# Performance work log

Measured on AMD Instinct MI355X. Metric: run time of the kernel, lower is better.

Reference implementation:

```python
import jax, jax.numpy as jnp
import numpy as np
import math

B, T, C = 2, 4096, 768
NH = 12
HS = C // NH

def setup_inputs() -> dict:
    key = jax.random.key(0)
    k1, k2, k3 = jax.random.split(key, 3)
    x = jax.random.normal(k1, (B, T, C), dtype=jnp.float32)
    w_attn = jax.random.normal(k2, (C, 3 * C), dtype=jnp.float32) * (1.0 / math.sqrt(C))
    w_proj = jax.random.normal(k3, (C, C), dtype=jnp.float32) * (1.0 / math.sqrt(C))
    return {"x": x, "w_attn": w_attn, "w_proj": w_proj}

def reference(x, w_attn, w_proj):
    b, t, c = x.shape
    qkv = x @ w_attn                      # [b, t, 3c]
    q, k, v = jnp.split(qkv, 3, axis=-1)
    # [b, nh, t, hs]
    q = q.reshape(b, t, NH, HS).transpose(0, 2, 1, 3)
    k = k.reshape(b, t, NH, HS).transpose(0, 2, 1, 3)
    v = v.reshape(b, t, NH, HS).transpose(0, 2, 1, 3)
    scores = jnp.einsum('bhqd,bhkd->bhqk', q, k) / math.sqrt(HS)
    causal = jnp.tril(jnp.ones((t, t), dtype=bool))
    scores = jnp.where(causal[None, None], scores, -jnp.inf)
    att = jax.nn.softmax(scores, axis=-1)  # dropout p=0 -> identity
    out = jnp.einsum('bhqk,bhkd->bhqd', att, v)
    out = out.transpose(0, 2, 1, 3).reshape(b, t, c)
    return out @ w_proj
```

## Files before the change

### kernel.cpp

```cpp
#include <hip/hip_runtime.h>
#include <hip/hip_bf16.h>
#include <stdint.h>

#define NB 2
#define NT 4096
#define NC 768
#define NHEAD 12
#define HS 64
#define MTOK (NB * NT)
#define C3 (3 * NC)

typedef __bf16 bf16x8 __attribute__((ext_vector_type(8)));
typedef float f32x4 __attribute__((ext_vector_type(4)));
typedef float f32x16 __attribute__((ext_vector_type(16)));

#define KSCALE_LOG2E 0.18033688011f

__device__ __forceinline__ unsigned short f2bf(float f) {
  union { float f; uint32_t u; } v; v.f = f;
  uint32_t r = v.u + 0x7fffu + ((v.u >> 16) & 1u);
  return (unsigned short)(r >> 16);
}
__device__ __forceinline__ unsigned short bft(float f) {
  return (unsigned short)(__builtin_bit_cast(unsigned int, f) >> 16);
}
__device__ __forceinline__ uint32_t pack_bf2(float a, float b) {
  return (__builtin_bit_cast(uint32_t, b) & 0xffff0000u) |
         (__builtin_bit_cast(uint32_t, a) >> 16);
}

__device__ __forceinline__ void gload_lds16(const unsigned short* g, unsigned short* ldsbase) {
  __builtin_amdgcn_global_load_lds(
      (const __attribute__((address_space(1))) unsigned int*)g,
      (__attribute__((address_space(3))) unsigned int*)ldsbase, 16, 0, 0);
}

__device__ __forceinline__ f32x4 mfma16(bf16x8 a, bf16x8 b, f32x4 c) {
  return __builtin_amdgcn_mfma_f32_16x16x32_bf16(a, b, c, 0, 0, 0);
}
__device__ __forceinline__ f32x16 mfma32(bf16x8 a, bf16x8 b, f32x16 c) {
  return __builtin_amdgcn_mfma_f32_32x32x16_bf16(a, b, c, 0, 0, 0);
}

__global__ __launch_bounds__(256) void prep(
    const float* __restrict__ x, const float* __restrict__ wa, const float* __restrict__ wp,
    unsigned short* __restrict__ xb, unsigned short* __restrict__ waT,
    unsigned short* __restrict__ wpT) {
  const int bx = blockIdx.x;
  if (bx < 576) {
    __shared__ float tile[64][65];
    const float* src; unsigned short* dst;
    int srcN, dstN, k0, n0, qscale;
    if (bx < 432) {
      src = wa; dst = waT; srcN = C3; dstN = NC; qscale = 1;
      k0 = (bx / 36) * 64; n0 = (bx % 36) * 64;
    } else {
      const int t = bx - 432;
      src = wp; dst = wpT; srcN = NC; dstN = NC; qscale = 0;
      k0 = (t / 12) * 64; n0 = (t % 12) * 64;
    }
    const int tr = threadIdx.x >> 4;
    const int tc = (threadIdx.x & 15) * 4;
#pragma unroll
    for (int p = 0; p < 4; ++p) {
      const int r = p * 16 + tr;
      const float4 v = *reinterpret_cast<const float4*>(src + (size_t)(k0 + r) * srcN + n0 + tc);
      tile[r][tc + 0] = v.x; tile[r][tc + 1] = v.y;
      tile[r][tc + 2] = v.z; tile[r][tc + 3] = v.w;
    }
    __syncthreads();
#pragma unroll
    for (int p = 0; p < 4; ++p) {
      const int n = p * 16 + tr;
      const float sc = (qscale && (n0 + n) < NC) ? KSCALE_LOG2E : 1.0f;
      ushort4 o;
      o.x = f2bf(tile[tc + 0][n] * sc); o.y = f2bf(tile[tc + 1][n] * sc);
      o.z = f2bf(tile[tc + 2][n] * sc); o.w = f2bf(tile[tc + 3][n] * sc);
      *reinterpret_cast<ushort4*>(dst + (size_t)(n0 + n) * dstN + k0 + tc) = o;
    }
  } else {
    const int gid = (bx - 576) * 256 + threadIdx.x;
    const float4 v = reinterpret_cast<const float4*>(x)[gid];
    ushort4 o;
    o.x = f2bf(v.x); o.y = f2bf(v.y); o.z = f2bf(v.z); o.w = f2bf(v.w);
    reinterpret_cast<ushort4*>(xb)[gid] = o;
  }
}

template <int OUT_BF16>
__global__ __launch_bounds__(256) void gemm128(
    const unsigned short* __restrict__ A,
    const unsigned short* __restrict__ Bt,
    void* __restrict__ Cout,
    unsigned short* __restrict__ vT,
    int M, int N, int K) {
  __shared__ unsigned short smem[2 * 128 * 64];
  unsigned short* As = smem;
  unsigned short* Bs = smem + 128 * 64;

  const int tid = threadIdx.x;
  const int wave = tid >> 6;
  const int lane = tid & 63;
  const int li = lane & 15;
  const int lq = lane >> 4;
  const int wm = wave & 1;
  const int wn = wave >> 1;
  const int row0 = blockIdx.y * 128;
  const int col0 = blockIdx.x * 128;

  const int crow = lane >> 3;
  const int cchunk = ((lane & 7) ^ crow) * 8;

  f32x4 acc[4][4] = {};

  for (int k0 = 0; k0 < K; k0 += 64) {
#pragma unroll
    for (int i = 0; i < 4; ++i) {
      const int R = wave * 32 + i * 8;
      gload_lds16(A + (size_t)(row0 + R + crow) * K + k0 + cchunk, &As[R * 64]);
      gload_lds16(Bt + (size_t)(col0 + R + crow) * K + k0 + cchunk, &Bs[R * 64]);
    }
    __syncthreads();

#pragma unroll
    for (int ks = 0; ks < 2; ++ks) {
      bf16x8 af[4], bf[4];
#pragma unroll
      for (int f = 0; f < 4; ++f) {
        const int arow = wm * 64 + f * 16 + li;
        af[f] = *reinterpret_cast<const bf16x8*>(&As[arow * 64 + (((ks * 4 + lq) ^ (li & 7)) << 3)]);
        const int brow = wn * 64 + f * 16 + li;
        bf[f] = *reinterpret_cast<const bf16x8*>(&Bs[brow * 64 + (((ks * 4 + lq) ^ (li & 7)) << 3)]);
      }
#pragma unroll
      for (int fa = 0; fa < 4; ++fa)
#pragma unroll
        for (int fb = 0; fb < 4; ++fb)
          acc[fa][fb] = mfma16(af[fa], bf[fb], acc[fa][fb]);
    }
    __syncthreads();
  }

  if (OUT_BF16) {
    if (col0 >= 2 * NC) {
      const int b = row0 >> 12;
      const int t0r = row0 & (NT - 1);
      const int h0 = (col0 - 2 * NC) >> 6;
#pragma unroll
      for (int fa = 0; fa < 4; ++fa) {
#pragma unroll
        for (int fb = 0; fb < 4; ++fb) {
          const int cc = wn * 64 + fb * 16 + li;
#pragma unroll
          for (int r = 0; r < 4; ++r) {
            const int tt = wm * 64 + fa * 16 + lq * 4 + r;
            const int slot = cc * 16 + ((tt >> 3) ^ (cc & 15));
            smem[slot * 8 + (tt & 7)] = f2bf(acc[fa][fb][r]);
          }
        }
      }
      __syncthreads();
      const int ch = tid & 15;
#pragma unroll
      for (int j = 0; j < 8; ++j) {
        const int cc = (tid >> 4) + 16 * j;
        const uint4 v = *reinterpret_cast<const uint4*>(
            smem + (size_t)(cc * 16 + (ch ^ (cc & 15))) * 8);
        const int bh = b * NHEAD + h0 + (cc >> 6);
        const int d = cc & 63;
        *reinterpret_cast<uint4*>(vT + (size_t)bh * HS * NT + (size_t)d * NT + t0r + ch * 8) = v;
      }
    } else {
      unsigned short* Cb = (unsigned short*)Cout;
#pragma unroll
      for (int fa = 0; fa < 4; ++fa) {
        const int gr = row0 + wm * 64 + fa * 16 + lq * 4;
#pragma unroll
        for (int fb = 0; fb < 4; ++fb) {
          const int gc = col0 + wn * 64 + fb * 16 + li;
#pragma unroll
          for (int r = 0; r < 4; ++r)
            Cb[(size_t)(gr + r) * N + gc] = f2bf(acc[fa][fb][r]);
        }
      }
    }
  } else {
    float* Cf = (float*)Cout;
#pragma unroll
    for (int fa = 0; fa < 4; ++fa) {
      const int gr = row0 + wm * 64 + fa * 16 + lq * 4;
#pragma unroll
      for (int fb = 0; fb < 4; ++fb) {
        const int gc = col0 + wn * 64 + fb * 16 + li;
#pragma unroll
        for (int r = 0; r < 4; ++r)
          Cf[(size_t)(gr + r) * N + gc] = acc[fa][fb][r];
      }
    }
  }
}


__global__ __launch_bounds__(256) void attn(
    const unsigned short* __restrict__ qkv,
    const unsigned short* __restrict__ vT,
    float* __restrict__ Oacc,
    float* __restrict__ lacc,
    unsigned short* __restrict__ aob) {
  __shared__ unsigned short Ks[3][64 * 64];
  __shared__ unsigned short Vts[3][64 * 64];

  const int tid = threadIdx.x;
  const int wave = tid >> 6;
  const int lane = tid & 63;
  const int l31 = lane & 31;
  const int lh = lane >> 5;
  const int sw = l31 & 7;

  const int bid = (int)blockIdx.x;
  const int w = (bid & 7) * 144 + (bid >> 3);
  const int grp = w / 48;
  const int idx = w - grp * 48;
  const int b = grp / 12;
  const int h = grp - b * 12;
  int qi, tauS, tauE, part, split;
  if (idx < 32) {
    split = 1;
    part = idx & 1;
    qi = 31 - (idx >> 1);
    const int nt = 2 * qi + 2;
    if (part) { tauS = nt >> 1; tauE = nt; }
    else      { tauS = 0;       tauE = nt >> 1; }
  } else {
    split = 0; part = 0;
    qi = 47 - idx;
    tauS = 0; tauE = 2 * qi + 2;
  }
  const int q0 = qi * 128;
  const int bh = b * NHEAD + h;

  const size_t baseQ = (size_t)b * NT * C3 + (size_t)h * HS;
  const size_t baseK = baseQ + NC;
  const unsigned short* kq = qkv + baseK;
  const unsigned short* vbase = vT + (size_t)bh * HS * NT;

  const int qw = q0 + wave * 32;
  const int qtok = qw + l31;

  bf16x8 bq[4];
#pragma unroll
  for (int ks = 0; ks < 4; ++ks)
    bq[ks] = *reinterpret_cast<const bf16x8*>(
        qkv + baseQ + (size_t)(qw + l31) * C3 + ks * 16 + lh * 8);

  bf16x8 vones;
#pragma unroll
  for (int i = 0; i < 8; ++i) vones[i] = (__bf16)1.0f;

  f32x16 o0 = {}, o1 = {}, la = {};

  const int grow = lane >> 3;
  const int gch = (lane & 7) ^ grow;
  const int wr0 = wave * 8;
  const int wr1 = wave * 8 + 32;

#define STAGE(TAU, BUFI)                                                        \
  do {                                                                          \
    const int t0s_ = (TAU) * 64;                                                \
    gload_lds16(kq + (size_t)(t0s_ + wr0 + grow) * C3 + gch * 8,                \
                &Ks[BUFI][wr0 * 64]);                                           \
    gload_lds16(kq + (size_t)(t0s_ + wr1 + grow) * C3 + gch * 8,                \
                &Ks[BUFI][wr1 * 64]);                                           \
    gload_lds16(vbase + (size_t)(wr0 + grow) * NT + t0s_ + gch * 8,             \
                &Vts[BUFI][wr0 * 64]);                                          \
    gload_lds16(vbase + (size_t)(wr1 + grow) * NT + t0s_ + gch * 8,             \
                &Vts[BUFI][wr1 * 64]);                                          \
  } while (0)

#define EXP_PACK(ST, KBLK, DOMASK)                                             \
  do {                                                                         \
    const int kb_ = t0 + (KBLK) * 32 + 4 * lh;                                 \
    float p_[16];                                                              \
    _Pragma("unroll") for (int r = 0; r < 16; ++r) {                           \
      float v_ = (ST)[r];                                                      \
      if (DOMASK) {                                                            \
        const int kt_ = kb_ + (r & 3) + 8 * (r >> 2);                          \
        if (kt_ > qtok) v_ = -INFINITY;                                        \
      }                                                                        \
      p_[r] = __builtin_amdgcn_exp2f(v_);                                      \
    }                                                                          \
    _Pragma("unroll") for (int s = 0; s < 2; ++s) {                            \
      uint32_t a_ = pack_bf2(p_[8 * s + 0], p_[8 * s + 1]);                    \
      uint32_t b_ = pack_bf2(p_[8 * s + 2], p_[8 * s + 3]);                    \
      uint32_t c_ = pack_bf2(p_[8 * s + 4], p_[8 * s + 5]);                    \
      uint32_t d_ = pack_bf2(p_[8 * s + 6], p_[8 * s + 7]);                    \
      asm("v_permlane32_swap_b32 %0, %1" : "+v"(a_), "+v"(c_));                \
      asm("v_permlane32_swap_b32 %0, %1" : "+v"(b_), "+v"(d_));                \
      union { uint32_t u[4]; bf16x8 v8; } pu_;                                 \
      pu_.u[0] = a_; pu_.u[1] = b_; pu_.u[2] = c_; pu_.u[3] = d_;              \
      pa[2 * (KBLK) + s] = pu_.v8;                                             \
    }                                                                          \
  } while (0)

#define PV_STEP(KS)                                                            \
  do {                                                                         \
    const int off_ = ((((KS) * 2 + lh) ^ sw) << 3);                            \
    const bf16x8 bv0_ =                                                        \
        *reinterpret_cast<const bf16x8*>(Vc + (size_t)l31 * 64 + off_);        \
    const bf16x8 bv1_ =                                                        \
        *reinterpret_cast<const bf16x8*>(Vc + (size_t)(32 + l31) * 64 + off_); \
    la = mfma32(pa[KS], vones, la);                                            \
    o0 = mfma32(pa[KS], bv0_, o0);                                             \
    o1 = mfma32(pa[KS], bv1_, o1);                                             \
  } while (0)

  STAGE(tauS, 0);
  STAGE(tauS + 1, 1);

  int cur = 0;
  for (int tau = tauS; tau < tauE; ++tau) {
    const int t0 = tau * 64;
    if (tau + 1 < tauE) asm volatile("s_waitcnt vmcnt(4)" ::: "memory");
    else                asm volatile("s_waitcnt vmcnt(0)" ::: "memory");
    __builtin_amdgcn_s_barrier();
    __builtin_amdgcn_sched_barrier(0);
    if (tau + 2 < tauE) {
      int nb = cur + 2; if (nb >= 3) nb -= 3;
      STAGE(tau + 2, nb);
    }

    const unsigned short* Kc = Ks[cur];
    const unsigned short* Vc = Vts[cur];

    if (t0 <= qw + 31) {
      const bool act1 = (t0 + 32 <= qw + 31);
      const bool m0 = (t0 + 31 > qw);
      const bool m1 = (t0 + 63 > qw);

      f32x16 st0 = {}, st1 = {};
      __builtin_amdgcn_s_setprio(1);
#pragma unroll
      for (int ks = 0; ks < 4; ++ks) {
        const bf16x8 ka = *reinterpret_cast<const bf16x8*>(
            Kc + (size_t)l31 * 64 + (((ks * 2 + lh) ^ sw) << 3));
        st0 = mfma32(ka, bq[ks], st0);
      }
      if (act1) {
#pragma unroll
        for (int ks = 0; ks < 4; ++ks) {
          const bf16x8 ka = *reinterpret_cast<const bf16x8*>(
              Kc + (size_t)(32 + l31) * 64 + (((ks * 2 + lh) ^ sw) << 3));
          st1 = mfma32(ka, bq[ks], st1);
        }
      }
      __builtin_amdgcn_s_setprio(0);

      bf16x8 pa[4];
      EXP_PACK(st0, 0, m0);
      if (act1) EXP_PACK(st1, 1, m1);

      __builtin_amdgcn_s_setprio(1);
      PV_STEP(0); PV_STEP(1);
      if (act1) { PV_STEP(2); PV_STEP(3); }
      __builtin_amdgcn_s_setprio(0);
    }
    ++cur; if (cur == 3) cur = 0;
  }
#undef STAGE
#undef EXP_PACK
#undef PV_STEP

  if (split) {
    float* lrow = lacc + (size_t)bh * NT;
#pragma unroll
    for (int r = 0; r < 16; ++r) {
      const int q = qw + (r & 3) + 8 * (r >> 2) + 4 * lh;
      const int srow = part ? (q - 2048) : q;
      if (l31 == 0) lrow[srow] = la[r];
      float* orow = Oacc + ((size_t)b * NT + srow) * NC + h * HS;
      orow[l31] = o0[r];
      orow[32 + l31] = o1[r];
    }
  } else {
#pragma unroll
    for (int r = 0; r < 16; ++r) {
      const int q = qw + (r & 3) + 8 * (r >> 2) + 4 * lh;
      const float inv = 1.0f / la[r];
      unsigned short* orow = aob + ((size_t)b * NT + q) * NC + h * HS;
      orow[l31] = bft(o0[r] * inv);
      orow[32 + l31] = bft(o1[r] * inv);
    }
  }
}

__global__ __launch_bounds__(256) void finalize(
    const float* __restrict__ Oacc, const float* __restrict__ lacc,
    unsigned short* __restrict__ aob) {
  const int idx4 = (blockIdx.x * 256 + threadIdx.x);
  if (idx4 >= NB * (NT / 2) * NC / 4) return;
  const int idx = idx4 * 4;
  const int rowp = idx / NC;
  const int cc = idx - rowp * NC;
  const int b = rowp >> 11;
  const int t = (NT / 2) + (rowp & 2047);
  const int h = cc >> 6;
  const float* lrow = lacc + (size_t)(b * NHEAD + h) * NT;
  const float inv = 1.0f / (lrow[t] + lrow[t - 2048]);
  const size_t base0 = ((size_t)b * NT + t) * NC + cc;
  const size_t base1 = ((size_t)b * NT + (t - 2048)) * NC + cc;
  const float4 v0 = *reinterpret_cast<const float4*>(Oacc + base0);
  const float4 v1 = *reinterpret_cast<const float4*>(Oacc + base1);
  ushort4 o;
  o.x = bft((v0.x + v1.x) * inv); o.y = bft((v0.y + v1.y) * inv);
  o.z = bft((v0.z + v1.z) * inv); o.w = bft((v0.w + v1.w) * inv);
  *reinterpret_cast<ushort4*>(aob + base0) = o;
}

extern "C" void kernel_launch(void* const* d_in, const int* in_sizes, int n_in,
                              void* d_out, int out_size, void* d_ws, size_t ws_size,
                              hipStream_t stream) {
  const float* x = (const float*)d_in[0];
  const float* w_attn = (const float*)d_in[1];
  const float* w_proj = (const float*)d_in[2];
  float* outp = (float*)d_out;

  char* w = (char*)d_ws;
  float* Oacc = (float*)w;
  unsigned short* xb = (unsigned short*)w;
  unsigned short* waT = xb + (size_t)MTOK * NC;
  float* lacc = Oacc + (size_t)MTOK * NC;
  unsigned short* qkvb = (unsigned short*)(lacc + (size_t)NB * NHEAD * NT);
  unsigned short* aob  = qkvb + (size_t)MTOK * C3;
  unsigned short* vTb  = aob + (size_t)MTOK * NC;
  unsigned short* wpT  = vTb + (size_t)MTOK * NC;

  prep<<<576 + MTOK * NC / 4 / 256, 256, 0, stream>>>(x, w_attn, w_proj, xb, waT, wpT);

  gemm128<1><<<dim3(C3 / 128, MTOK / 128), 256, 0, stream>>>(xb, waT, qkvb, vTb, MTOK, C3, NC);

  attn<<<1152, 256, 0, stream>>>(qkvb, vTb, Oacc, lacc, aob);

  finalize<<<(NB * (NT / 2) * NC / 4 + 255) / 256, 256, 0, stream>>>(Oacc, lacc, aob);

  gemm128<0><<<dim3(NC / 128, MTOK / 128), 256, 0, stream>>>(aob, wpT, outp, nullptr, MTOK, NC, NC);
}
```

Before: 252.8 us.

## Rebalance attention work per XCD via lookup table and trim softmax packing

Replaces the arithmetic block-to-work mapping with a device lookup table. Each XCD now gets three fixed heads, and a balanced ordering interleaves split and unsplit query tiles so per-XCD load and K/V L2 locality improve. It also uses v_perm for bf16 packing, seeds the first MFMA with a zero constant instead of zero-initialised accumulators, and specialises the mask branch of the exp/pack step at compile time. The table ordering must cover every tile exactly once, and the duplicated branches grow code size.

```diff
diff --git a/kernel.cpp b/kernel.cpp
--- a/kernel.cpp
+++ b/kernel.cpp
@@ -25,8 +25,8 @@
   return (unsigned short)(__builtin_bit_cast(unsigned int, f) >> 16);
 }
 __device__ __forceinline__ uint32_t pack_bf2(float a, float b) {
-  return (__builtin_bit_cast(uint32_t, b) & 0xffff0000u) |
-         (__builtin_bit_cast(uint32_t, a) >> 16);
+  return __builtin_amdgcn_perm(__builtin_bit_cast(uint32_t, a),
+                               __builtin_bit_cast(uint32_t, b), 0x03020706u);
 }
 
 __device__ __forceinline__ void gload_lds16(const unsigned short* g, unsigned short* ldsbase) {
@@ -201,6 +201,11 @@
 }
 
 
+__device__ const uint8_t g_items[48] = {
+  95,127,15, 94,126, 93,125,14, 92,124, 91,123,13, 90,122, 89,121,12, 88,120,
+  87,119,11, 86,118, 85,117,10, 84,116, 83,115,9, 82,114, 81,113,8, 80,112,
+  7,6,5,4,3,2,1,0};
+
 __global__ __launch_bounds__(256) void attn(
     const unsigned short* __restrict__ qkv,
     const unsigned short* __restrict__ vT,
@@ -218,26 +223,21 @@
   const int sw = l31 & 7;
 
   const int bid = (int)blockIdx.x;
-  const int w = (bid & 7) * 144 + (bid >> 3);
-  const int grp = w / 48;
-  const int idx = w - grp * 48;
+  const int xcd = bid & 7;
+  const int wl = bid >> 3;
+  const int grp = xcd * 3 + wl % 3;
+  const int e = (int)g_items[wl / 3];
+  const int qi = e & 31;
+  const int part = (e >> 5) & 1;
+  const int split = e >> 6;
+  const int nt = 2 * qi + 2;
+  int tauS, tauE;
+  if (split) { if (part) { tauS = nt >> 1; tauE = nt; } else { tauS = 0; tauE = nt >> 1; } }
+  else       { tauS = 0; tauE = nt; }
   const int b = grp / 12;
   const int h = grp - b * 12;
-  int qi, tauS, tauE, part, split;
-  if (idx < 32) {
-    split = 1;
-    part = idx & 1;
-    qi = 31 - (idx >> 1);
-    const int nt = 2 * qi + 2;
-    if (part) { tauS = nt >> 1; tauE = nt; }
-    else      { tauS = 0;       tauE = nt >> 1; }
-  } else {
-    split = 0; part = 0;
-    qi = 47 - idx;
-    tauS = 0; tauE = 2 * qi + 2;
-  }
   const int q0 = qi * 128;
-  const int bh = b * NHEAD + h;
+  const int bh = grp;
 
   const size_t baseQ = (size_t)b * NT * C3 + (size_t)h * HS;
   const size_t baseK = baseQ + NC;
@@ -258,6 +258,7 @@
   for (int i = 0; i < 8; ++i) vones[i] = (__bf16)1.0f;
 
   f32x16 o0 = {}, o1 = {}, la = {};
+  const f32x16 zf = {};
 
   const int grow = lane >> 3;
   const int gch = (lane & 7) ^ grow;
@@ -337,17 +338,27 @@
       const bool m0 = (t0 + 31 > qw);
       const bool m1 = (t0 + 63 > qw);
 
-      f32x16 st0 = {}, st1 = {};
+      f32x16 st0, st1;
       __builtin_amdgcn_s_setprio(1);
-#pragma unroll
-      for (int ks = 0; ks < 4; ++ks) {
+      {
+        const bf16x8 ka0 = *reinterpret_cast<const bf16x8*>(
+            Kc + (size_t)l31 * 64 + ((lh ^ sw) << 3));
+        st0 = mfma32(ka0, bq[0], zf);
+      }
+#pragma unroll
+      for (int ks = 1; ks < 4; ++ks) {
         const bf16x8 ka = *reinterpret_cast<const bf16x8*>(
             Kc + (size_t)l31 * 64 + (((ks * 2 + lh) ^ sw) << 3));
         st0 = mfma32(ka, bq[ks], st0);
       }
       if (act1) {
-#pragma unroll
-        for (int ks = 0; ks < 4; ++ks) {
+        {
+          const bf16x8 ka0 = *reinterpret_cast<const bf16x8*>(
+              Kc + (size_t)(32 + l31) * 64 + ((lh ^ sw) << 3));
+          st1 = mfma32(ka0, bq[0], zf);
+        }
+#pragma unroll
+        for (int ks = 1; ks < 4; ++ks) {
           const bf16x8 ka = *reinterpret_cast<const bf16x8*>(
               Kc + (size_t)(32 + l31) * 64 + (((ks * 2 + lh) ^ sw) << 3));
           st1 = mfma32(ka, bq[ks], st1);
@@ -356,8 +367,10 @@
       __builtin_amdgcn_s_setprio(0);
 
       bf16x8 pa[4];
-      EXP_PACK(st0, 0, m0);
-      if (act1) EXP_PACK(st1, 1, m1);
+      if (m0) EXP_PACK(st0, 0, 1); else EXP_PACK(st0, 0, 0);
+      if (act1) {
+        if (m1) EXP_PACK(st1, 1, 1); else EXP_PACK(st1, 1, 0);
+      }
 
       __builtin_amdgcn_s_setprio(1);
       PV_STEP(0); PV_STEP(1);
```

Measured after the change: 242.3 us. 4.2% less time.
